# Optimization experiments

Measured on AMD Instinct MI355X. Metric: run time of the kernel, lower is better.

The kernel has to match this reference:

```python
import jax, jax.numpy as jnp
import numpy as np
import math

B, H, W = 4, 256, 256
S = 256          # num_superpixels
ZD = 128         # z_dim
GC = 256         # g_channels
NBLK = 8


def setup_inputs() -> dict:
    key = jax.random.key(0)
    ks = jax.random.split(key, 12)
    rn = lambda k, shp, s=1.0: jax.random.normal(k, shp, jnp.float32) * s
    return {
        "z": rn(ks[0], (B, ZD)),
        "images": rn(ks[1], (B, 3, H, W)),
        "segments": jax.random.randint(ks[2], (B, H, W), 0, S).astype(jnp.int32),
        # row-stochastic-ish adjacency scale keeps 8 propagations stable
        "A": rn(ks[3], (B, S, S), 1.0 / math.sqrt(S)),
        # WSConv2d weights: init N(0,1); forward multiplies input by sqrt(2/(in*k*k))
        "proj_w": rn(ks[4], (GC, 3 + ZD)), "proj_b": jnp.zeros((GC,), jnp.float32),
        "blk_proj_w": rn(ks[5], (NBLK, GC, GC)), "blk_proj_b": jnp.zeros((NBLK, GC), jnp.float32),
        "ada1_w": rn(ks[6], (NBLK, 2 * GC, GC)), "ada1_b": jnp.zeros((NBLK, 2 * GC), jnp.float32),
        "ada2_w": rn(ks[7], (NBLK, 2 * GC, 2 * GC)), "ada2_b": jnp.zeros((NBLK, 2 * GC), jnp.float32),
        # plain Conv2d 3x3 layers in upsample head
        "up1_w": rn(ks[8], (GC // 2, GC, 3, 3), 0.02), "up1_b": jnp.zeros((GC // 2,), jnp.float32),
        "up2_w": rn(ks[9], (3, GC // 2, 3, 3), 0.02), "up2_b": jnp.zeros((3,), jnp.float32),
    }


def _ws1x1(x, w, b):
    # WSConv2d with 1x1 kernel over node dim: x [B,Cin,S] -> [B,Cout,S]
    scale = math.sqrt(2.0 / w.shape[1])
    return jnp.einsum('oc,bcs->bos', w, x) * scale + b[None, :, None]


def _conv3(x, w, b):
    y = jax.lax.conv_general_dilated(x, w, (1, 1), 'SAME',
                                     dimension_numbers=('NCHW', 'OIHW', 'NCHW'))
    return y + b[None, :, None, None]


def _forward(z, images, A, proj_w, proj_b, blk_proj_w, blk_proj_b,
             ada1_w, ada1_b, ada2_w, ada2_b, up1_w, up1_b, up2_w, up2_b,
             segments):
    Bn, _, Hn, Wn = images.shape
    N = Hn * Wn
    flat = images.reshape(Bn, 3, N)            # [B,3,N]
    seg = segments.reshape(Bn, N)              # [B,N] int

    # superpixel mean pooling (math of one_hot^T @ flat / counts, as segment-sum)
    seg_sum = jax.vmap(lambda f, s: jax.ops.segment_sum(f, s, num_segments=S))(
        flat.transpose(0, 2, 1), seg)          # [B,S,3]
    counts = jax.vmap(lambda s: jax.ops.segment_sum(
        jnp.ones(s.shape, jnp.float32), s, num_segments=S))(seg)  # [B,S]
    feats = seg_sum / (counts[..., None] + 1e-6)

    z_rep = jnp.broadcast_to(z[:, None, :], (Bn, S, ZD))
    x = jnp.concatenate([feats, z_rep], axis=2).transpose(0, 2, 1)  # [B,3+ZD,S]
    x = _ws1x1(x, proj_w, proj_b)                                   # [B,GC,S]

    for i in range(NBLK):
        h = _ws1x1(x, blk_proj_w[i], blk_proj_b[i])
        # A @ feat : out[b,c,i] = sum_j A[b,i,j] h[b,c,j]
        h = jnp.einsum('bij,bcj->bci', A, h)
        # AdaIN: style from global mean over nodes
        m = h.mean(axis=2, keepdims=True)                    # [B,GC,1]
        s1 = jax.nn.leaky_relu(_ws1x1(m, ada1_w[i], ada1_b[i]), 0.2)
        style = _ws1x1(s1, ada2_w[i], ada2_b[i])             # [B,2GC,1]
        gamma, beta = jnp.split(style, 2, axis=1)
        h = gamma * h + beta
        x = jax.nn.leaky_relu(h, 0.2)                        # dropout=0 (eval)

    # broadcast superpixel feats back to pixels (math of one_hot @ sup_feats)
    sup_feats = x.transpose(0, 2, 1)                         # [B,S,GC]
    pix = jnp.take_along_axis(sup_feats, seg[:, :, None].astype(jnp.int32), axis=1)  # [B,N,GC]
    pix = pix.transpose(0, 2, 1).reshape(Bn, GC, Hn, Wn)

    y = jax.nn.leaky_relu(_conv3(pix, up1_w, up1_b), 0.2)
    y = _conv3(y, up2_w, up2_b)                              # [B,3,H,W]
    # InstanceNorm2d(3), affine=False, eps=1e-5
    mu = y.mean((2, 3), keepdims=True)
    var = y.var((2, 3), keepdims=True)
    y = (y - mu) / jnp.sqrt(var + 1e-5)
    return jnp.tanh(y)


def reference(z, images, segments, A, proj_w, proj_b, blk_proj_w, blk_proj_b,
              ada1_w, ada1_b, ada2_w, ada2_b, up1_w, up1_b, up2_w, up2_b):
    return _forward(z, images, A, proj_w, proj_b, blk_proj_w, blk_proj_b,
                    ada1_w, ada1_b, ada2_w, ada2_b, up1_w, up1_b, up2_w, up2_b,
                    segments)
```

## Files before the change

### kernel.cpp

```cpp
#include <hip/hip_runtime.h>
#include <cmath>

#define BB 4
#define SS 256
#define ZDIM 128
#define GCH 256
#define NBLKS 8
#define NPIX 65536
#define U1C 128

__device__ __forceinline__ float lrelu(float x){ return x >= 0.f ? x : 0.2f*x; }

__global__ void k_pool(const float* __restrict__ img, const int* __restrict__ seg,
                       float* __restrict__ segsum, float* __restrict__ counts){
  __shared__ float ls[SS*4];
  int t = threadIdx.x;
  for(int j=t;j<SS*4;j+=256) ls[j]=0.f;
  __syncthreads();
  int b = blockIdx.x >> 6;
  int base = blockIdx.x*1024;
  for(int it=0; it<4; it++){
    int idx = base + it*256 + t;
    int n = idx & (NPIX-1);
    int s = seg[idx];
    atomicAdd(&ls[s*4+0], img[(b*3+0)*NPIX+n]);
    atomicAdd(&ls[s*4+1], img[(b*3+1)*NPIX+n]);
    atomicAdd(&ls[s*4+2], img[(b*3+2)*NPIX+n]);
    atomicAdd(&ls[s*4+3], 1.0f);
  }
  __syncthreads();
  for(int j=t;j<SS*4;j+=256){
    int s = j>>2, c = j&3;
    float vv = ls[j];
    if(vv != 0.f){
      if(c<3) atomicAdd(&segsum[(b*SS+s)*3+c], vv);
      else    atomicAdd(&counts[b*SS+s], vv);
    }
  }
}

__global__ __launch_bounds__(256) void k_prep(const float* __restrict__ A,
        const float* __restrict__ w1, const float* __restrict__ w2,
        float* __restrict__ At2, float* __restrict__ wT, float* __restrict__ w2t){
  int bid = blockIdx.x;
  if(bid < 256){
    __shared__ float t[32][33];
    int b = bid >> 6;
    int bx = (bid & 7)*32, by = ((bid >> 3) & 7)*32;
    int lx = threadIdx.x & 31, ly4 = (threadIdx.x >> 5)*4;
    #pragma unroll
    for(int r=0;r<4;r++)
      t[ly4+r][lx] = A[(b<<16) + ((by+ly4+r)<<8) + bx + lx];
    __syncthreads();
    #pragma unroll
    for(int r=0;r<4;r++){
      int jj = bx + ly4 + r;
      int i  = by + lx;
      At2[(b<<16) + ((jj>>2)<<10) + (i<<2) + (jj&3)] = t[lx][ly4+r];
    }
  } else {
    int idx = (bid-256)*256 + threadIdx.x;
    if(idx < 294912){
      int o = idx & 127; int r = idx >> 7; int c = r & 255; int k = r >> 8;
      wT[idx] = w1[(o*GCH + c)*9 + k];
    } else if(idx < 294912 + 3456){
      int t2 = idx - 294912;
      int cc = t2 & 7;
      int oc = (t2 >> 3) % 3;
      int sg = (t2 / 24) & 3;
      int g  = (t2 / 96) & 3;
      int k  = t2 / 384;
      w2t[t2] = w2[oc*1152 + (g*32 + sg*8 + cc)*9 + k];
    }
  }
}

__global__ __launch_bounds__(256) void k_x0(const float* __restrict__ segsum,
        const float* __restrict__ counts, const float* __restrict__ z,
        const float* __restrict__ pw, const float* __restrict__ pb,
        float sc, float4* __restrict__ xp2){
  int og = blockIdx.x;
  int b  = blockIdx.y;
  int i  = threadIdx.x;
  float cnt = counts[b*SS+i] + 1e-6f;
  float f0 = segsum[(b*SS+i)*3+0]/cnt;
  float f1 = segsum[(b*SS+i)*3+1]/cnt;
  float f2 = segsum[(b*SS+i)*3+2]/cnt;
  const float* zb = z + b*ZDIM;
  float vals[4];
  #pragma unroll
  for(int oo=0;oo<4;oo++){
    int o = og*4 + oo;
    const float* wr = pw + o*131;
    float acc = wr[0]*f0 + wr[1]*f1 + wr[2]*f2;
    #pragma unroll 8
    for(int j=0;j<ZDIM;j++) acc += wr[3+j]*zb[j];
    vals[oo] = acc*sc + pb[o];
  }
  float4 o4 = {vals[0], vals[1], vals[2], vals[3]};
  xp2[(b*64+og)*256 + i] = o4;
}

__global__ __launch_bounds__(512) void k_gemm(const float4* __restrict__ xp2,
        const float* __restrict__ bw, const float* __restrict__ bb,
        const float4* __restrict__ At2, float sc,
        float* __restrict__ h2, float* __restrict__ m){
  int c0 = blockIdx.x*4;
  int b  = blockIdx.y;
  int tid = threadIdx.x;
  int j  = tid & 255;
  int half = tid >> 8;
  int ch0 = c0 + half*2;
  __shared__ float4 wl4[4][64];
  __shared__ float4 h1l4[4][66];
  __shared__ float red[4][4];
  for(int t = tid; t < 1024; t += 512){
    int row = t >> 8, jj = t & 255;
    ((float*)&wl4[row][0])[jj] = bw[(c0+row)*GCH + jj];
  }
  __syncthreads();
  const float4* xb = xp2 + (b*64)*256 + j;
  float a0 = 0.f, a1 = 0.f;
  int r0i = half*2, r1i = half*2+1;
  #pragma unroll 8
  for(int kg=0;kg<64;kg++){
    float4 x = xb[kg*256];
    float4 w0 = wl4[r0i][kg];
    float4 w1 = wl4[r1i][kg];
    a0 += w0.x*x.x + w0.y*x.y + w0.z*x.z + w0.w*x.w;
    a1 += w1.x*x.x + w1.y*x.y + w1.z*x.z + w1.w*x.w;
  }
  ((float*)&h1l4[r0i][0])[j] = a0*sc + bb[ch0];
  ((float*)&h1l4[r1i][0])[j] = a1*sc + bb[ch0+1];
  __syncthreads();
  const float4* ab = At2 + (b*64)*256 + j;
  float r0 = 0.f, r1 = 0.f;
  #pragma unroll 8
  for(int kg=0;kg<64;kg++){
    float4 a = ab[kg*256];
    float4 h0 = h1l4[r0i][kg];
    float4 h1 = h1l4[r1i][kg];
    r0 += a.x*h0.x + a.y*h0.y + a.z*h0.z + a.w*h0.w;
    r1 += a.x*h1.x + a.y*h1.y + a.z*h1.z + a.w*h1.w;
  }
  h2[(b*GCH+ch0)*SS + j]   = r0;
  h2[(b*GCH+ch0+1)*SS + j] = r1;
  float s0 = r0, s1v = r1;
  for(int off=32; off; off>>=1){ s0 += __shfl_down(s0,off); s1v += __shfl_down(s1v,off); }
  int w3 = (tid >> 6) & 3;
  if((j&63)==0){ red[r0i][w3] = s0; red[r1i][w3] = s1v; }
  __syncthreads();
  if(tid < 4)
    m[b*GCH + c0 + tid] =
      (red[tid][0]+red[tid][1]+red[tid][2]+red[tid][3])*(1.f/256.f);
}

__global__ __launch_bounds__(512) void k_s12(const float* __restrict__ m,
        const float* __restrict__ a1w, const float* __restrict__ a1b,
        const float* __restrict__ a2w, const float* __restrict__ a2b,
        const float* __restrict__ h2, float sc1, float sc2,
        float4* __restrict__ xp2){
  int q = blockIdx.x;
  int tid = threadIdx.x;
  int lane = tid & 63, wv = tid >> 6;
  int grp = lane >> 3, ll = lane & 7;
  __shared__ float4 ml4[256];
  __shared__ float s1l[4][512];
  __shared__ float gbl[4][16];
  if(tid < 256) ml4[tid] = ((const float4*)m)[tid];
  __syncthreads();
  #pragma unroll 2
  for(int pass=0; pass<8; pass++){
    int row = wv*64 + pass*8 + grp;
    const float4* ar = (const float4*)(a1w + row*GCH) + ll;
    float p0=0.f,p1=0.f,p2=0.f,p3=0.f;
    #pragma unroll
    for(int j=0;j<8;j++){
      float4 w4 = ar[j*8];
      float4 m0 = ml4[0*64 + j*8 + ll];
      float4 m1 = ml4[1*64 + j*8 + ll];
      float4 m2 = ml4[2*64 + j*8 + ll];
      float4 m3 = ml4[3*64 + j*8 + ll];
      p0 += w4.x*m0.x + w4.y*m0.y + w4.z*m0.z + w4.w*m0.w;
      p1 += w4.x*m1.x + w4.y*m1.y + w4.z*m1.z + w4.w*m1.w;
      p2 += w4.x*m2.x + w4.y*m2.y + w4.z*m2.z + w4.w*m2.w;
      p3 += w4.x*m3.x + w4.y*m3.y + w4.z*m3.z + w4.w*m3.w;
    }
    #pragma unroll
    for(int off=1; off<8; off<<=1){
      p0 += __shfl_xor(p0,off); p1 += __shfl_xor(p1,off);
      p2 += __shfl_xor(p2,off); p3 += __shfl_xor(p3,off);
    }
    if(ll == 0){
      float bv = a1b[row];
      int sidx = ((row & 7) << 6) + (row >> 3);
      s1l[0][sidx] = lrelu(p0*sc1 + bv);
      s1l[1][sidx] = lrelu(p1*sc1 + bv);
      s1l[2][sidx] = lrelu(p2*sc1 + bv);
      s1l[3][sidx] = lrelu(p3*sc1 + bv);
    }
  }
  __syncthreads();
  float sA[4][8];
  #pragma unroll
  for(int b=0;b<4;b++)
    #pragma unroll
    for(int j=0;j<8;j++) sA[b][j] = s1l[b][j*64 + lane];
  #pragma unroll
  for(int r=0;r<2;r++){
    int ridx = wv*2 + r;
    int cc = ridx & 7;
    int t = (ridx < 8) ? (q*8 + cc) : (256 + q*8 + cc);
    const float* wr = a2w + t*512 + lane*8;
    float4 wa = *(const float4*)wr;
    float4 wb4 = *(const float4*)(wr+4);
    float p0 = wa.x*sA[0][0]+wa.y*sA[0][1]+wa.z*sA[0][2]+wa.w*sA[0][3]
             + wb4.x*sA[0][4]+wb4.y*sA[0][5]+wb4.z*sA[0][6]+wb4.w*sA[0][7];
    float p1 = wa.x*sA[1][0]+wa.y*sA[1][1]+wa.z*sA[1][2]+wa.w*sA[1][3]
             + wb4.x*sA[1][4]+wb4.y*sA[1][5]+wb4.z*sA[1][6]+wb4.w*sA[1][7];
    float p2 = wa.x*sA[2][0]+wa.y*sA[2][1]+wa.z*sA[2][2]+wa.w*sA[2][3]
             + wb4.x*sA[2][4]+wb4.y*sA[2][5]+wb4.z*sA[2][6]+wb4.w*sA[2][7];
    float p3 = wa.x*sA[3][0]+wa.y*sA[3][1]+wa.z*sA[3][2]+wa.w*sA[3][3]
             + wb4.x*sA[3][4]+wb4.y*sA[3][5]+wb4.z*sA[3][6]+wb4.w*sA[3][7];
    for(int off=32; off; off>>=1){
      p0 += __shfl_xor(p0,off); p1 += __shfl_xor(p1,off);
      p2 += __shfl_xor(p2,off); p3 += __shfl_xor(p3,off);
    }
    if(lane < 4){
      float p = lane==0 ? p0 : lane==1 ? p1 : lane==2 ? p2 : p3;
      gbl[lane][ridx] = p*sc2 + a2b[t];
    }
  }
  __syncthreads();
  int j = tid & 255;
  int cg2 = tid >> 8;
  int cbase = q*8 + cg2*4;
  int cg = cbase >> 2;
  #pragma unroll
  for(int b=0;b<4;b++){
    float4 o;
    o.x = lrelu(gbl[b][cg2*4+0]*h2[(b*GCH + cbase+0)*SS + j] + gbl[b][8+cg2*4+0]);
    o.y = lrelu(gbl[b][cg2*4+1]*h2[(b*GCH + cbase+1)*SS + j] + gbl[b][8+cg2*4+1]);
    o.z = lrelu(gbl[b][cg2*4+2]*h2[(b*GCH + cbase+2)*SS + j] + gbl[b][8+cg2*4+2]);
    o.w = lrelu(gbl[b][cg2*4+3]*h2[(b*GCH + cbase+3)*SS + j] + gbl[b][8+cg2*4+3]);
    xp2[(b*64 + cg)*256 + j] = o;
  }
}

__global__ __launch_bounds__(256) void k_v(const float4* __restrict__ xp2,
        const float4* __restrict__ wT4, float4* __restrict__ v4){
  int s0 = blockIdx.x*16;
  int k  = blockIdx.y;
  int b  = blockIdx.z;
  int tid = threadIdx.x;
  __shared__ float4 wl[64][33];
  __shared__ float xft[256][17];
  for(int t = tid; t < 1024; t += 256){
    int cg = t >> 4, si = t & 15;
    float4 xv = xp2[(b*64 + cg)*256 + s0 + si];
    xft[cg*4+0][si] = xv.x;
    xft[cg*4+1][si] = xv.y;
    xft[cg*4+2][si] = xv.z;
    xft[cg*4+3][si] = xv.w;
  }
  int og = tid & 31, sh = tid >> 5;
  const float4* wb = wT4 + (size_t)k*GCH*32;
  float4 a0 = {0.f,0.f,0.f,0.f}, a1 = {0.f,0.f,0.f,0.f};
  for(int ct=0; ct<4; ct++){
    __syncthreads();
    for(int t = tid; t < 2048; t += 256){
      int cc = t>>5, o = t&31;
      wl[cc][o] = wb[(ct*64+cc)*32 + o];
    }
    __syncthreads();
    #pragma unroll 4
    for(int cc=0;cc<64;cc++){
      float4 w = wl[cc][og];
      int c = ct*64+cc;
      float x0v = xft[c][sh];
      float x1v = xft[c][8+sh];
      a0.x += w.x*x0v; a0.y += w.y*x0v; a0.z += w.z*x0v; a0.w += w.w*x0v;
      a1.x += w.x*x1v; a1.y += w.y*x1v; a1.z += w.z*x1v; a1.w += w.w*x1v;
    }
  }
  size_t base = (size_t)(b*9+k)*SS + s0;
  v4[(base + sh)*32 + og]     = a0;
  v4[(base + 8 + sh)*32 + og] = a1;
}

__global__ __launch_bounds__(256) void k_conv(const float4* __restrict__ v4,
        const int* __restrict__ seg, const float4* __restrict__ b14,
        const float* __restrict__ w2t, float* __restrict__ y2){
  __shared__ float4 y1t4[100*9];
  __shared__ int   segl[144];
  __shared__ float part[768];
  int bid = blockIdx.x;
  int x = bid & 7;
  int b = x >> 1;
  int sub = ((bid >> 3) << 1) + (x & 1);
  int g = sub & 3;
  int tile = sub >> 2;
  int x0p = (tile & 31)*8, y0p = (tile >> 5)*8;
  int tid = threadIdx.x;
  if(tid < 144){
    int r = tid/12, cc = tid%12;
    int gy = y0p - 2 + r, gx = x0p - 2 + cc;
    segl[tid] = (gy>=0 && gy<256 && gx>=0 && gx<256) ? seg[(b*256+gy)*256+gx] : -1;
  }
  __syncthreads();
  int o4 = tid & 7;
  const float4* vb = v4 + (size_t)(b*9)*SS*32 + g*8 + o4;
  float4 bias = b14[g*8 + o4];
  bool interior = (x0p >= 8 && x0p <= 240 && y0p >= 8 && y0p <= 240);
  if(interior){
    for(int task = tid; task < 800; task += 256){
      int pp = task >> 3;
      int py = pp/10, px = pp - py*10;
      float4 acc = bias;
      #pragma unroll
      for(int k=0;k<9;k++){
        int sidx = segl[(py + k/3)*12 + (px + k%3)];
        float4 vv = vb[(k*SS + sidx)*32];
        acc.x += vv.x; acc.y += vv.y; acc.z += vv.z; acc.w += vv.w;
      }
      float4 val;
      val.x = lrelu(acc.x); val.y = lrelu(acc.y);
      val.z = lrelu(acc.z); val.w = lrelu(acc.w);
      y1t4[pp*9 + o4] = val;
    }
  } else {
    for(int task = tid; task < 800; task += 256){
      int pp = task >> 3;
      int py = pp/10, px = pp - py*10;
      int gy = y0p - 1 + py, gx = x0p - 1 + px;
      bool pix_ok = (gy>=0 && gy<256 && gx>=0 && gx<256);
      float4 acc = bias;
      #pragma unroll
      for(int k=0;k<9;k++){
        int sidx = segl[(py + k/3)*12 + (px + k%3)];
        int sidx0 = sidx < 0 ? 0 : sidx;
        float msk = sidx < 0 ? 0.f : 1.f;
        float4 vv = vb[(k*SS + sidx0)*32];
        acc.x += msk*vv.x; acc.y += msk*vv.y; acc.z += msk*vv.z; acc.w += msk*vv.w;
      }
      float4 val;
      val.x = pix_ok ? lrelu(acc.x) : 0.f;
      val.y = pix_ok ? lrelu(acc.y) : 0.f;
      val.z = pix_ok ? lrelu(acc.z) : 0.f;
      val.w = pix_ok ? lrelu(acc.w) : 0.f;
      y1t4[pp*9 + o4] = val;
    }
  }
  __syncthreads();
  int pxo = tid & 63, sg = tid >> 6;
  int sgu = __builtin_amdgcn_readfirstlane(sg);
  const float* wk0 = w2t + (g*4 + sgu)*24;
  int ty = pxo >> 3, tx = pxo & 7;
  float p0=0.f,p1=0.f,p2=0.f;
  #pragma unroll
  for(int k=0;k<9;k++){
    int pp0 = (ty + k/3)*10 + (tx + k%3);
    float4 ya = y1t4[pp0*9 + sgu*2];
    float4 yb = y1t4[pp0*9 + sgu*2 + 1];
    const float* wk = wk0 + k*384;
    p0 += wk[0]*ya.x + wk[1]*ya.y + wk[2]*ya.z + wk[3]*ya.w
        + wk[4]*yb.x + wk[5]*yb.y + wk[6]*yb.z + wk[7]*yb.w;
    p1 += wk[8]*ya.x + wk[9]*ya.y + wk[10]*ya.z + wk[11]*ya.w
        + wk[12]*yb.x + wk[13]*yb.y + wk[14]*yb.z + wk[15]*yb.w;
    p2 += wk[16]*ya.x + wk[17]*ya.y + wk[18]*ya.z + wk[19]*ya.w
        + wk[20]*yb.x + wk[21]*yb.y + wk[22]*yb.z + wk[23]*yb.w;
  }
  part[tid]     = p0;
  part[256+tid] = p1;
  part[512+tid] = p2;
  __syncthreads();
  if(tid < 64){
    float s0 = part[tid]    +part[tid+64]    +part[tid+128]    +part[tid+192];
    float s1 = part[256+tid]+part[256+tid+64]+part[256+tid+128]+part[256+tid+192];
    float s2 = part[512+tid]+part[512+tid+64]+part[512+tid+128]+part[512+tid+192];
    int gy = y0p + (tid>>3), gx = x0p + (tid&7);
    int nidx = gy*256+gx;
    atomicAdd(&y2[(b*3+0)*NPIX+nidx], s0);
    atomicAdd(&y2[(b*3+1)*NPIX+nidx], s1);
    atomicAdd(&y2[(b*3+2)*NPIX+nidx], s2);
  }
}

__global__ void k_stats(const float* __restrict__ y2, double* __restrict__ stats){
  int bc = blockIdx.x;
  int chunk = blockIdx.y;
  const float* p = y2 + (size_t)bc*NPIX + chunk*8192;
  int t = threadIdx.x;
  double s=0.0, q=0.0;
  for(int i=t;i<8192;i+=256){ double vv = (double)p[i]; s+=vv; q+=vv*vv; }
  __shared__ double rs[256], rq[256];
  rs[t]=s; rq[t]=q; __syncthreads();
  for(int st=128; st; st>>=1){ if(t<st){rs[t]+=rs[t+st]; rq[t]+=rq[t+st];} __syncthreads(); }
  if(t==0){ atomicAdd(&stats[bc*2], rs[0]); atomicAdd(&stats[bc*2+1], rq[0]); }
}

__global__ void k_norm(const float* __restrict__ y2, const double* __restrict__ stats,
                       float* __restrict__ out){
  int bu = (blockIdx.x*256) >> 16;
  double mu  = stats[bu*2+0] * (1.0/65536.0);
  double ex2 = stats[bu*2+1] * (1.0/65536.0);
  double var = ex2 - mu*mu;
  float inv = (float)(1.0/sqrt(var + 1e-5));
  float mf = (float)mu;
  int idx = blockIdx.x*256+threadIdx.x;
  out[idx] = tanhf((y2[idx]-mf)*inv);
}

extern "C" void kernel_launch(void* const* d_in, const int* in_sizes, int n_in,
                              void* d_out, int out_size, void* d_ws, size_t ws_size,
                              hipStream_t stream) {
  const float* z   = (const float*)d_in[0];
  const float* img = (const float*)d_in[1];
  const int*   seg = (const int*)d_in[2];
  const float* A   = (const float*)d_in[3];
  const float* pw  = (const float*)d_in[4];
  const float* pb  = (const float*)d_in[5];
  const float* bw  = (const float*)d_in[6];
  const float* bb  = (const float*)d_in[7];
  const float* a1w = (const float*)d_in[8];
  const float* a1b = (const float*)d_in[9];
  const float* a2w = (const float*)d_in[10];
  const float* a2b = (const float*)d_in[11];
  const float* w1  = (const float*)d_in[12];
  const float* b1  = (const float*)d_in[13];
  const float* w2  = (const float*)d_in[14];
  const float* b2  = (const float*)d_in[15]; (void)b2;
  float* out = (float*)d_out;

  float* ws = (float*)d_ws;
  float* segsum = ws;
  float* counts = ws + 3072;
  float* m      = ws + 4096;
  double* stats = (double*)(ws + 5120);
  float* xp2 = ws + 5248;
  float* h2  = xp2 + 262144;
  float* At2 = h2 + 262144;
  float* wT  = At2 + 262144;
  float* v   = wT + 294912;
  float* y2  = v + 1179648;
  float* w2t = y2 + 786432;

  hipMemsetAsync(ws, 0, 5248*sizeof(float), stream);
  hipMemsetAsync(y2, 0, 786432*sizeof(float), stream);

  float sProj = (float)sqrt(2.0/131.0);
  float s256  = (float)sqrt(2.0/256.0);
  float s512  = (float)sqrt(2.0/512.0);

  k_pool<<<256, 256, 0, stream>>>(img, seg, segsum, counts);
  k_prep<<<256 + 1166, 256, 0, stream>>>(A, w1, w2, At2, wT, w2t);
  k_x0  <<<dim3(64,4), 256, 0, stream>>>(segsum, counts, z, pw, pb, sProj,
                                         (float4*)xp2);

  for(int blk=0; blk<NBLKS; blk++){
    k_gemm<<<dim3(64,4), 512, 0, stream>>>((const float4*)xp2,
                                           bw + blk*GCH*GCH, bb + blk*GCH,
                                           (const float4*)At2, s256, h2, m);
    k_s12 <<<32, 512, 0, stream>>>(m, a1w + blk*512*GCH, a1b + blk*512,
                                   a2w + blk*512*512, a2b + blk*512,
                                   h2, s256, s512, (float4*)xp2);
  }

  k_v   <<<dim3(16,9,4), 256, 0, stream>>>((const float4*)xp2, (const float4*)wT,
                                           (float4*)v);
  k_conv<<<16384, 256, 0, stream>>>((const float4*)v, seg, (const float4*)b1, w2t, y2);
  k_stats<<<dim3(12,8), 256, 0, stream>>>(y2, stats);
  k_norm<<<3072, 256, 0, stream>>>(y2, stats, out);
}
```

Before: 372.9 us.

## Merge pool and prep kernels, split-K gemm, two float4 per conv1 gather

```diff
diff --git a/kernel.cpp b/kernel.cpp
--- a/kernel.cpp
+++ b/kernel.cpp
@@ -11,43 +11,43 @@
 
 __device__ __forceinline__ float lrelu(float x){ return x >= 0.f ? x : 0.2f*x; }
 
-__global__ void k_pool(const float* __restrict__ img, const int* __restrict__ seg,
-                       float* __restrict__ segsum, float* __restrict__ counts){
-  __shared__ float ls[SS*4];
-  int t = threadIdx.x;
-  for(int j=t;j<SS*4;j+=256) ls[j]=0.f;
-  __syncthreads();
-  int b = blockIdx.x >> 6;
-  int base = blockIdx.x*1024;
-  for(int it=0; it<4; it++){
-    int idx = base + it*256 + t;
-    int n = idx & (NPIX-1);
-    int s = seg[idx];
-    atomicAdd(&ls[s*4+0], img[(b*3+0)*NPIX+n]);
-    atomicAdd(&ls[s*4+1], img[(b*3+1)*NPIX+n]);
-    atomicAdd(&ls[s*4+2], img[(b*3+2)*NPIX+n]);
-    atomicAdd(&ls[s*4+3], 1.0f);
-  }
-  __syncthreads();
-  for(int j=t;j<SS*4;j+=256){
-    int s = j>>2, c = j&3;
-    float vv = ls[j];
-    if(vv != 0.f){
-      if(c<3) atomicAdd(&segsum[(b*SS+s)*3+c], vv);
-      else    atomicAdd(&counts[b*SS+s], vv);
-    }
-  }
-}
-
-__global__ __launch_bounds__(256) void k_prep(const float* __restrict__ A,
+__global__ __launch_bounds__(256) void k_pp(const float* __restrict__ img,
+        const int* __restrict__ seg, float* __restrict__ segsum,
+        float* __restrict__ counts, const float* __restrict__ A,
         const float* __restrict__ w1, const float* __restrict__ w2,
         float* __restrict__ At2, float* __restrict__ wT, float* __restrict__ w2t){
   int bid = blockIdx.x;
+  int tid = threadIdx.x;
   if(bid < 256){
+    __shared__ float ls[SS*4];
+    for(int j=tid;j<SS*4;j+=256) ls[j]=0.f;
+    __syncthreads();
+    int b = bid >> 6;
+    int base = bid*1024;
+    for(int it=0; it<4; it++){
+      int idx = base + it*256 + tid;
+      int n = idx & (NPIX-1);
+      int s = seg[idx];
+      atomicAdd(&ls[s*4+0], img[(b*3+0)*NPIX+n]);
+      atomicAdd(&ls[s*4+1], img[(b*3+1)*NPIX+n]);
+      atomicAdd(&ls[s*4+2], img[(b*3+2)*NPIX+n]);
+      atomicAdd(&ls[s*4+3], 1.0f);
+    }
+    __syncthreads();
+    for(int j=tid;j<SS*4;j+=256){
+      int s = j>>2, c = j&3;
+      float vv = ls[j];
+      if(vv != 0.f){
+        if(c<3) atomicAdd(&segsum[(b*SS+s)*3+c], vv);
+        else    atomicAdd(&counts[b*SS+s], vv);
+      }
+    }
+  } else if(bid < 512){
     __shared__ float t[32][33];
-    int b = bid >> 6;
-    int bx = (bid & 7)*32, by = ((bid >> 3) & 7)*32;
-    int lx = threadIdx.x & 31, ly4 = (threadIdx.x >> 5)*4;
+    int sb = bid - 256;
+    int b = sb >> 6;
+    int bx = (sb & 7)*32, by = ((sb >> 3) & 7)*32;
+    int lx = tid & 31, ly4 = (tid >> 5)*4;
     #pragma unroll
     for(int r=0;r<4;r++)
       t[ly4+r][lx] = A[(b<<16) + ((by+ly4+r)<<8) + bx + lx];
@@ -59,7 +59,7 @@
       At2[(b<<16) + ((jj>>2)<<10) + (i<<2) + (jj&3)] = t[lx][ly4+r];
     }
   } else {
-    int idx = (bid-256)*256 + threadIdx.x;
+    int idx = (bid-512)*256 + tid;
     if(idx < 294912){
       int o = idx & 127; int r = idx >> 7; int c = r & 255; int k = r >> 8;
       wT[idx] = w1[(o*GCH + c)*9 + k];
@@ -109,9 +109,9 @@
   int b  = blockIdx.y;
   int tid = threadIdx.x;
   int j  = tid & 255;
-  int half = tid >> 8;
-  int ch0 = c0 + half*2;
+  int h  = tid >> 8;
   __shared__ float4 wl4[4][64];
+  __shared__ float ps[8][260];
   __shared__ float4 h1l4[4][66];
   __shared__ float red[4][4];
   for(int t = tid; t < 1024; t += 512){
@@ -119,36 +119,69 @@
     ((float*)&wl4[row][0])[jj] = bw[(c0+row)*GCH + jj];
   }
   __syncthreads();
-  const float4* xb = xp2 + (b*64)*256 + j;
-  float a0 = 0.f, a1 = 0.f;
-  int r0i = half*2, r1i = half*2+1;
-  #pragma unroll 8
-  for(int kg=0;kg<64;kg++){
-    float4 x = xb[kg*256];
-    float4 w0 = wl4[r0i][kg];
-    float4 w1 = wl4[r1i][kg];
-    a0 += w0.x*x.x + w0.y*x.y + w0.z*x.z + w0.w*x.w;
-    a1 += w1.x*x.x + w1.y*x.y + w1.z*x.z + w1.w*x.w;
-  }
-  ((float*)&h1l4[r0i][0])[j] = a0*sc + bb[ch0];
-  ((float*)&h1l4[r1i][0])[j] = a1*sc + bb[ch0+1];
-  __syncthreads();
-  const float4* ab = At2 + (b*64)*256 + j;
-  float r0 = 0.f, r1 = 0.f;
-  #pragma unroll 8
-  for(int kg=0;kg<64;kg++){
-    float4 a = ab[kg*256];
-    float4 h0 = h1l4[r0i][kg];
-    float4 h1 = h1l4[r1i][kg];
-    r0 += a.x*h0.x + a.y*h0.y + a.z*h0.z + a.w*h0.w;
-    r1 += a.x*h1.x + a.y*h1.y + a.z*h1.z + a.w*h1.w;
-  }
-  h2[(b*GCH+ch0)*SS + j]   = r0;
-  h2[(b*GCH+ch0+1)*SS + j] = r1;
-  float s0 = r0, s1v = r1;
-  for(int off=32; off; off>>=1){ s0 += __shfl_down(s0,off); s1v += __shfl_down(s1v,off); }
-  int w3 = (tid >> 6) & 3;
-  if((j&63)==0){ red[r0i][w3] = s0; red[r1i][w3] = s1v; }
+  {
+    const float4* xb = xp2 + (b*64 + h*32)*256 + j;
+    float a0=0.f, a1=0.f, a2=0.f, a3=0.f;
+    #pragma unroll 8
+    for(int kg=0; kg<32; kg++){
+      float4 x  = xb[kg*256];
+      float4 w0 = wl4[0][h*32+kg];
+      float4 w1v= wl4[1][h*32+kg];
+      float4 w2v= wl4[2][h*32+kg];
+      float4 w3 = wl4[3][h*32+kg];
+      a0 += w0.x*x.x + w0.y*x.y + w0.z*x.z + w0.w*x.w;
+      a1 += w1v.x*x.x + w1v.y*x.y + w1v.z*x.z + w1v.w*x.w;
+      a2 += w2v.x*x.x + w2v.y*x.y + w2v.z*x.z + w2v.w*x.w;
+      a3 += w3.x*x.x + w3.y*x.y + w3.z*x.z + w3.w*x.w;
+    }
+    ps[0+h][j] = a0; ps[2+h][j] = a1; ps[4+h][j] = a2; ps[6+h][j] = a3;
+  }
+  __syncthreads();
+  if(tid < 256){
+    #pragma unroll
+    for(int ch=0;ch<4;ch++){
+      float vv = (ps[ch*2][tid] + ps[ch*2+1][tid])*sc + bb[c0+ch];
+      ((float*)&h1l4[ch][0])[tid] = vv;
+    }
+  }
+  __syncthreads();
+  {
+    const float4* ab = At2 + (b*64 + h*32)*256 + j;
+    float r0=0.f, r1=0.f, r2=0.f, r3=0.f;
+    #pragma unroll 8
+    for(int kg=0; kg<32; kg++){
+      float4 a  = ab[kg*256];
+      float4 h0 = h1l4[0][h*32+kg];
+      float4 h1 = h1l4[1][h*32+kg];
+      float4 h2v= h1l4[2][h*32+kg];
+      float4 h3 = h1l4[3][h*32+kg];
+      r0 += a.x*h0.x + a.y*h0.y + a.z*h0.z + a.w*h0.w;
+      r1 += a.x*h1.x + a.y*h1.y + a.z*h1.z + a.w*h1.w;
+      r2 += a.x*h2v.x + a.y*h2v.y + a.z*h2v.z + a.w*h2v.w;
+      r3 += a.x*h3.x + a.y*h3.y + a.z*h3.z + a.w*h3.w;
+    }
+    ps[0+h][j] = r0; ps[2+h][j] = r1; ps[4+h][j] = r2; ps[6+h][j] = r3;
+  }
+  __syncthreads();
+  float rr0=0.f, rr1=0.f, rr2=0.f, rr3=0.f;
+  if(tid < 256){
+    rr0 = ps[0][tid]+ps[1][tid];
+    rr1 = ps[2][tid]+ps[3][tid];
+    rr2 = ps[4][tid]+ps[5][tid];
+    rr3 = ps[6][tid]+ps[7][tid];
+    h2[(b*GCH+c0+0)*SS + tid] = rr0;
+    h2[(b*GCH+c0+1)*SS + tid] = rr1;
+    h2[(b*GCH+c0+2)*SS + tid] = rr2;
+    h2[(b*GCH+c0+3)*SS + tid] = rr3;
+  }
+  for(int off=32; off; off>>=1){
+    rr0 += __shfl_down(rr0,off); rr1 += __shfl_down(rr1,off);
+    rr2 += __shfl_down(rr2,off); rr3 += __shfl_down(rr3,off);
+  }
+  if(tid < 256 && (tid & 63)==0){
+    int w3 = tid >> 6;
+    red[0][w3]=rr0; red[1][w3]=rr1; red[2][w3]=rr2; red[3][w3]=rr3;
+  }
   __syncthreads();
   if(tid < 4)
     m[b*GCH + c0 + tid] =
@@ -308,47 +341,58 @@
     segl[tid] = (gy>=0 && gy<256 && gx>=0 && gx<256) ? seg[(b*256+gy)*256+gx] : -1;
   }
   __syncthreads();
-  int o4 = tid & 7;
-  const float4* vb = v4 + (size_t)(b*9)*SS*32 + g*8 + o4;
-  float4 bias = b14[g*8 + o4];
+  int o2 = tid & 3;
+  const float4* vb = v4 + (size_t)(b*9)*SS*32 + g*8 + o2*2;
+  float4 biasA = b14[g*8 + o2*2];
+  float4 biasB = b14[g*8 + o2*2 + 1];
   bool interior = (x0p >= 8 && x0p <= 240 && y0p >= 8 && y0p <= 240);
   if(interior){
-    for(int task = tid; task < 800; task += 256){
-      int pp = task >> 3;
+    for(int task = tid; task < 400; task += 256){
+      int pp = task >> 2;
       int py = pp/10, px = pp - py*10;
-      float4 acc = bias;
+      float4 aA = biasA, aB = biasB;
       #pragma unroll
       for(int k=0;k<9;k++){
         int sidx = segl[(py + k/3)*12 + (px + k%3)];
-        float4 vv = vb[(k*SS + sidx)*32];
-        acc.x += vv.x; acc.y += vv.y; acc.z += vv.z; acc.w += vv.w;
+        const float4* pv = vb + (k*SS + sidx)*32;
+        float4 vA = pv[0], vB = pv[1];
+        aA.x += vA.x; aA.y += vA.y; aA.z += vA.z; aA.w += vA.w;
+        aB.x += vB.x; aB.y += vB.y; aB.z += vB.z; aB.w += vB.w;
       }
-      float4 val;
-      val.x = lrelu(acc.x); val.y = lrelu(acc.y);
-      val.z = lrelu(acc.z); val.w = lrelu(acc.w);
-      y1t4[pp*9 + o4] = val;
+      float4 valA, valB;
+      valA.x = lrelu(aA.x); valA.y = lrelu(aA.y); valA.z = lrelu(aA.z); valA.w = lrelu(aA.w);
+      valB.x = lrelu(aB.x); valB.y = lrelu(aB.y); valB.z = lrelu(aB.z); valB.w = lrelu(aB.w);
+      y1t4[pp*9 + o2*2]     = valA;
+      y1t4[pp*9 + o2*2 + 1] = valB;
     }
   } else {
-    for(int task = tid; task < 800; task += 256){
-      int pp = task >> 3;
+    for(int task = tid; task < 400; task += 256){
+      int pp = task >> 2;
       int py = pp/10, px = pp - py*10;
       int gy = y0p - 1 + py, gx = x0p - 1 + px;
       bool pix_ok = (gy>=0 && gy<256 && gx>=0 && gx<256);
-      float4 acc = bias;
+      float4 aA = biasA, aB = biasB;
       #pragma unroll
       for(int k=0;k<9;k++){
         int sidx = segl[(py + k/3)*12 + (px + k%3)];
         int sidx0 = sidx < 0 ? 0 : sidx;
         float msk = sidx < 0 ? 0.f : 1.f;
-        float4 vv = vb[(k*SS + sidx0)*32];
-        acc.x += msk*vv.x; acc.y += msk*vv.y; acc.z += msk*vv.z; acc.w += msk*vv.w;
+        const float4* pv = vb + (k*SS + sidx0)*32;
+        float4 vA = pv[0], vB = pv[1];
+        aA.x += msk*vA.x; aA.y += msk*vA.y; aA.z += msk*vA.z; aA.w += msk*vA.w;
+        aB.x += msk*vB.x; aB.y += msk*vB.y; aB.z += msk*vB.z; aB.w += msk*vB.w;
       }
-      float4 val;
-      val.x = pix_ok ? lrelu(acc.x) : 0.f;
-      val.y = pix_ok ? lrelu(acc.y) : 0.f;
-      val.z = pix_ok ? lrelu(acc.z) : 0.f;
-      val.w = pix_ok ? lrelu(acc.w) : 0.f;
-      y1t4[pp*9 + o4] = val;
+      float4 valA, valB;
+      valA.x = pix_ok ? lrelu(aA.x) : 0.f;
+      valA.y = pix_ok ? lrelu(aA.y) : 0.f;
+      valA.z = pix_ok ? lrelu(aA.z) : 0.f;
+      valA.w = pix_ok ? lrelu(aA.w) : 0.f;
+      valB.x = pix_ok ? lrelu(aB.x) : 0.f;
+      valB.y = pix_ok ? lrelu(aB.y) : 0.f;
+      valB.z = pix_ok ? lrelu(aB.z) : 0.f;
+      valB.w = pix_ok ? lrelu(aB.w) : 0.f;
+      y1t4[pp*9 + o2*2]     = valA;
+      y1t4[pp*9 + o2*2 + 1] = valB;
     }
   }
   __syncthreads();
@@ -452,8 +496,8 @@
   float s256  = (float)sqrt(2.0/256.0);
   float s512  = (float)sqrt(2.0/512.0);
 
-  k_pool<<<256, 256, 0, stream>>>(img, seg, segsum, counts);
-  k_prep<<<256 + 1166, 256, 0, stream>>>(A, w1, w2, At2, wT, w2t);
+  k_pp  <<<512 + 1166, 256, 0, stream>>>(img, seg, segsum, counts,
+                                         A, w1, w2, At2, wT, w2t);
   k_x0  <<<dim3(64,4), 256, 0, stream>>>(segsum, counts, z, pw, pb, sProj,
                                          (float4*)xp2);
 
```

Measured after the change: 371.3 us. About the same (-0.4%).
